# Optimization experiments

Hardware: AMD Instinct MI355X
Metric: run time of the kernel (lower is better)

Reference implementation:

```python
import jax, jax.numpy as jnp
import numpy as np

B, C, H, W = 4, 64, 64, 64  # x shape; mask is (B,1,8H,8W)


def _conv(x, w, pad=0):
    return jax.lax.conv_general_dilated(
        x, w, (1, 1), [(pad, pad), (pad, pad)],
        dimension_numbers=('NCHW', 'OIHW', 'NCHW'))


def _inorm(x, eps=1e-5):  # InstanceNorm2d, affine=False, biased var (torch default)
    mu = x.mean(axis=(2, 3), keepdims=True)
    var = x.var(axis=(2, 3), keepdims=True)
    return (x - mu) * jax.lax.rsqrt(var + eps)


def _forward(x, mask, kconv_w1, kconv_w2, fs_w1, fs_w2, fs_b2, fs_fuse_w):
    b, c, h, w = x.shape
    n = h * w
    # MaxPool2d(8,8) then binarize
    m = jax.lax.reduce_window(mask, -jnp.inf, jax.lax.max,
                              (1, 1, 8, 8), (1, 1, 8, 8), 'VALID')
    m = (m > 0).astype(x.dtype)
    back = 1.0 - m
    # ResidualBlock K_conv (shared for K and Q paths in original code)
    y = jax.nn.relu(_inorm(_conv(x, kconv_w1, pad=1)))
    y = _inorm(_conv(y, kconv_w2, pad=1))
    kx = jax.nn.relu(y + x)
    # L2-normalized K/Q over channel dim
    K = (kx * back).reshape(b, c, n)
    K = K / (jnp.linalg.norm(K, axis=1, keepdims=True) + 1e-8)
    Q = (kx * m).reshape(b, c, n)
    Q = Q / (jnp.linalg.norm(Q, axis=1, keepdims=True) + 1e-8)
    V = (x * back).reshape(b, c, n)
    # cosine-similarity score map, temperature 20
    score = jnp.einsum('bcq,bck->bqk', Q, K) * 20.0  # (b, n_q, n_k)
    qm = m.reshape(b, 1, n)      # query mask (foreground)
    km = back.reshape(b, 1, n)   # key mask (background)
    NEG = -1000000.0
    validx = score + (1.0 - km) * NEG + (1.0 - qm.transpose(0, 2, 1)) * NEG
    att = jax.nn.softmax(validx, axis=-1) * (qm.transpose(0, 2, 1) * km)
    # att_fore[b,c,q] = sum_k V[b,c,k] * att[b,q,k]
    att_fore = jnp.einsum('bck,bqk->bcq', V, att).reshape(b, c, h, w)
    # Fusion_score
    feat1 = _conv(jnp.concatenate([x * m, att_fore * m], axis=1), fs_w1)
    s = jax.nn.sigmoid(_conv(feat1, fs_w2) + fs_b2[None, :, None, None])
    fused = _conv(jnp.concatenate([x * m, att_fore * m * (1.0 - s)], axis=1), fs_fuse_w)
    fs_out = fused * m + x * (1.0 - m)
    out = fs_out * m + x * (1.0 - m)
    # visualization attention mask
    visatt = att.sum(axis=1).reshape(b, 1, h, w)
    attmask = jnp.repeat(jnp.repeat(visatt, 8, axis=2), 8, axis=3)  # nearest upsample x8
    attmask = attmask / attmask.max()
    return out, attmask


def setup_inputs() -> dict:
    key = jax.random.key(0)
    ks = jax.random.split(key, 8)

    def wgt(k, shape, fan_in):
        return jax.random.normal(k, shape, jnp.float32) / np.sqrt(fan_in)

    x = jax.random.normal(ks[0], (B, C, H, W), jnp.float32)
    # sparse foreground mask so maxpool(8x8)>0 yields a mixed fg/bg mask
    mask = (jax.random.uniform(ks[1], (B, 1, H * 8, W * 8)) < 0.01).astype(jnp.float32)
    return dict(
        x=x, mask=mask,
        kconv_w1=wgt(ks[2], (C, C, 3, 3), C * 9),
        kconv_w2=wgt(ks[3], (C, C, 3, 3), C * 9),
        fs_w1=wgt(ks[4], (C, 2 * C, 1, 1), 2 * C),
        fs_w2=wgt(ks[5], (C, C, 1, 1), C),
        fs_b2=jnp.zeros((C,), jnp.float32),
        fs_fuse_w=wgt(ks[6], (C, 2 * C, 1, 1), 2 * C),
    )


def reference(x, mask, kconv_w1, kconv_w2, fs_w1, fs_w2, fs_b2, fs_fuse_w):
    return _forward(x, mask, kconv_w1, kconv_w2, fs_w1, fs_w2, fs_b2, fs_fuse_w)
```

## Files before the change

### kernel.cpp

```cpp
#include <hip/hip_runtime.h>
#include <hip/hip_bf16.h>

typedef __hip_bfloat16 bf16;
typedef __attribute__((ext_vector_type(8))) short short8;
typedef __attribute__((ext_vector_type(4))) float f32x4;
typedef __attribute__((ext_vector_type(16))) float f32x16;

#define BB 4
#define CC 64
#define NN 4096
#define MH 512
#define MW 512
#define LS 72

#define WB_AFC  ((size_t)0)
#define WB_DEN  ((size_t)4194304)
#define WB_VIS  ((size_t)4259840)
#define WB_QIX  ((size_t)4325376)
#define WB_KIX  ((size_t)4390912)
#define WB_MFL  ((size_t)4456448)
#define WB_CNT  ((size_t)4472832)
#define WB_STAT ((size_t)4472896)
#define WB_WT1  ((size_t)4476992)
#define WB_WT2  ((size_t)4550720)
#define WB_WFB  ((size_t)4624448)

__device__ __forceinline__ float b2f(bf16 v) { return __bfloat162float(v); }
__device__ __forceinline__ float us2f(unsigned short u) { return __uint_as_float(((unsigned)u) << 16); }
__device__ __forceinline__ unsigned short f2bu(float f) {
  bf16 h = __float2bfloat16(f);
  return *(unsigned short*)&h;
}

__global__ __launch_bounds__(256) void k_maxpool(const float* __restrict__ mask,
                                                 unsigned char* __restrict__ mfl,
                                                 float* __restrict__ vis,
                                                 float* __restrict__ gstat,
                                                 unsigned int* __restrict__ vmaxb) {
  int g = blockIdx.x * 256 + threadIdx.x;
  int o = g >> 2, sub = g & 3;
  int b = o >> 12, p = o & 4095;
  int py = p >> 6, px = p & 63;
  const float* mb = mask + (size_t)b * MH * MW + (py * 8 + sub * 2) * MW + px * 8;
  float mx = 0.f;
  #pragma unroll
  for (int dy = 0; dy < 2; ++dy) {
    const float4* r4 = (const float4*)(mb + dy * MW);
    float4 a = r4[0], c = r4[1];
    mx = fmaxf(mx, fmaxf(fmaxf(a.x, a.y), fmaxf(a.z, a.w)));
    mx = fmaxf(mx, fmaxf(fmaxf(c.x, c.y), fmaxf(c.z, c.w)));
  }
  mx = fmaxf(mx, __shfl_xor(mx, 1));
  mx = fmaxf(mx, __shfl_xor(mx, 2));
  if (sub == 0) {
    mfl[o] = (mx > 0.f) ? 1 : 0;
    vis[o] = 0.f;
  }
  if (g < 1024) gstat[g] = 0.f;
  if (g == 0) vmaxb[0] = 0u;
}

__global__ __launch_bounds__(64) void k_compact(const unsigned char* __restrict__ mfl,
                                                int* __restrict__ qidx, int* __restrict__ kidx,
                                                int* __restrict__ nq, int* __restrict__ nk) {
  int b = blockIdx.x, lane = threadIdx.x;
  int qb = 0, kb = 0;
  for (int it = 0; it < 64; ++it) {
    int p = it * 64 + lane;
    bool f = mfl[b * NN + p] != 0;
    unsigned long long bal = __ballot(f);
    int before = __popcll(bal & ((1ULL << lane) - 1ULL));
    if (f)  qidx[b * NN + qb + before] = p;
    if (!f) kidx[b * NN + kb + (lane - before)] = p;
    int cnt = __popcll(bal);
    qb += cnt; kb += 64 - cnt;
  }
  if (lane == 0) { nq[b] = qb; nk[b] = kb; }
}

__global__ __launch_bounds__(256) void k_xT(const float* __restrict__ x,
                                            unsigned short* __restrict__ xt) {
  int b = blockIdx.x >> 6, p0 = (blockIdx.x & 63) * 64;
  __shared__ float lx[64][65];
  int t = threadIdx.x;
  const float* xb = x + (size_t)b * CC * NN + p0;
  for (int idx = t; idx < 4096; idx += 256) {
    int c = idx >> 6, j = idx & 63;
    lx[j][c] = xb[c * NN + j];
  }
  __syncthreads();
  unsigned short* xo = xt + ((size_t)b * NN + p0) * 64;
  for (int idx = t; idx < 2048; idx += 256) {
    int j = idx >> 5, c2 = (idx & 31) * 2;
    ushort2 w2;
    w2.x = f2bu(lx[j][c2]);
    w2.y = f2bu(lx[j][c2 + 1]);
    *(ushort2*)&xo[j * 64 + c2] = w2;
  }
}

__global__ __launch_bounds__(256) void k_wprep(const float* __restrict__ w1,
                                               const float* __restrict__ w2,
                                               const float* __restrict__ fw1,
                                               const float* __restrict__ fw2,
                                               const float* __restrict__ fwf,
                                               unsigned short* __restrict__ wT1,
                                               unsigned short* __restrict__ wT2,
                                               unsigned short* __restrict__ wfb) {
  int i = blockIdx.x * 256 + threadIdx.x;
  if (i < 36864) {
    int tap = i >> 12;
    int rem = i & 4095;
    int co = rem >> 6, ci = rem & 63;
    int src = (co * 64 + ci) * 9 + tap;
    wT1[i] = f2bu(w1[src]);
    wT2[i] = f2bu(w2[src]);
  } else if (i < 57344) {
    int j = i - 36864;
    if (j < 8192)       wfb[j] = f2bu(fw1[j]);
    else if (j < 12288) wfb[j] = f2bu(fw2[j - 8192]);
    else                wfb[j] = f2bu(fwf[j - 12288]);
  }
}

template <bool NORM_IN>
__global__ __launch_bounds__(256) void k_convm(const unsigned short* __restrict__ src,
                                               const unsigned short* __restrict__ wT,
                                               const float* __restrict__ insum,
                                               const float* __restrict__ insq,
                                               unsigned short* __restrict__ dst,
                                               float* __restrict__ gsum,
                                               float* __restrict__ gsq) {
  int b = blockIdx.y;
  int r = blockIdx.x;
  __shared__ unsigned short bx[198 * LS];
  __shared__ float nmean[64], ninv[64];
  int t = threadIdx.x;
  if (NORM_IN) {
    if (t < 64) {
      float m = insum[b * 64 + t] * (1.f / NN);
      float v = fmaxf(insq[b * 64 + t] * (1.f / NN) - m * m, 0.f);
      nmean[t] = m; ninv[t] = rsqrtf(v + 1e-5f);
    }
    __syncthreads();
  }
  const unsigned short* sb = src + (size_t)b * NN * 64;
  for (int idx = t; idx < 198 * 8; idx += 256) {
    int row = idx >> 3, c8 = (idx & 7) * 8;
    int dy = row / 66;
    int cx = row - dy * 66 - 1;
    int rr = r + dy - 1;
    uint4 v = make_uint4(0u, 0u, 0u, 0u);
    if ((unsigned)rr < 64u && (unsigned)cx < 64u) {
      v = *(const uint4*)(sb + ((size_t)(rr * 64 + cx)) * 64 + c8);
      if (NORM_IN) {
        unsigned short* e = (unsigned short*)&v;
        #pragma unroll
        for (int j = 0; j < 8; ++j)
          e[j] = f2bu(fmaxf((us2f(e[j]) - nmean[c8 + j]) * ninv[c8 + j], 0.f));
      }
    }
    *(uint4*)&bx[row * LS + c8] = v;
  }
  __syncthreads();
  int lane = t & 63;
  int quad = lane >> 4, col = lane & 15;
  int qw = (t >> 6) * 16;
  f32x4 acc[4] = {{0.f,0.f,0.f,0.f},{0.f,0.f,0.f,0.f},{0.f,0.f,0.f,0.f},{0.f,0.f,0.f,0.f}};
  #pragma unroll
  for (int tap = 0; tap < 9; ++tap) {
    int dy = tap / 3, dx = tap - dy * 3 - 1;
    const unsigned short* wrow = wT + ((size_t)tap * 64 + qw + col) * 64;
    short8 a0 = *(const short8*)(wrow + quad * 8);
    short8 a1 = *(const short8*)(wrow + 32 + quad * 8);
    int rbase = dy * 66 + dx + 1;
    #pragma unroll
    for (int nt = 0; nt < 4; ++nt) {
      int row = rbase + nt * 16 + col;
      short8 b0 = *(const short8*)&bx[row * LS + quad * 8];
      short8 b1 = *(const short8*)&bx[row * LS + 32 + quad * 8];
      acc[nt] = __builtin_amdgcn_mfma_f32_16x16x32_bf16(a0, b0, acc[nt], 0, 0, 0);
      acc[nt] = __builtin_amdgcn_mfma_f32_16x16x32_bf16(a1, b1, acc[nt], 0, 0, 0);
    }
  }
  #pragma unroll
  for (int rr = 0; rr < 4; ++rr) {
    float s1 = acc[0][rr] + acc[1][rr] + acc[2][rr] + acc[3][rr];
    float s2 = acc[0][rr]*acc[0][rr] + acc[1][rr]*acc[1][rr]
             + acc[2][rr]*acc[2][rr] + acc[3][rr]*acc[3][rr];
    s1 += __shfl_xor(s1, 1); s2 += __shfl_xor(s2, 1);
    s1 += __shfl_xor(s1, 2); s2 += __shfl_xor(s2, 2);
    s1 += __shfl_xor(s1, 4); s2 += __shfl_xor(s2, 4);
    s1 += __shfl_xor(s1, 8); s2 += __shfl_xor(s2, 8);
    if (col == 0) {
      int co = qw + quad * 4 + rr;
      atomicAdd(&gsum[b * 64 + co], s1);
      atomicAdd(&gsq[b * 64 + co], s2);
    }
  }
  __syncthreads();
  #pragma unroll
  for (int nt = 0; nt < 4; ++nt)
    #pragma unroll
    for (int rr = 0; rr < 4; ++rr)
      bx[(nt * 16 + col) * LS + qw + quad * 4 + rr] = f2bu(acc[nt][rr]);
  __syncthreads();
  unsigned short* db = dst + ((size_t)b * NN + r * 64) * 64;
  for (int idx = t; idx < 512; idx += 256) {
    int px = idx >> 3, c8 = (idx & 7) * 8;
    *(uint4*)(db + (size_t)px * 64 + c8) = *(const uint4*)&bx[px * LS + c8];
  }
}

__global__ __launch_bounds__(256) void k_knorm(unsigned short* __restrict__ kxt,
                                               const unsigned short* __restrict__ xt,
                                               const float* __restrict__ gsum,
                                               const float* __restrict__ gsq,
                                               float* __restrict__ afc,
                                               float* __restrict__ den) {
  int b = blockIdx.x >> 6;
  int p0 = (blockIdx.x & 63) * 64;
  __shared__ float m2[64], i2[64];
  int t = threadIdx.x;
  if (t < 64) {
    float m = gsum[b * 64 + t] * (1.f / NN);
    float v = fmaxf(gsq[b * 64 + t] * (1.f / NN) - m * m, 0.f);
    m2[t] = m; i2[t] = rsqrtf(v + 1e-5f);
  }
  size_t gid = (size_t)blockIdx.x * 256 + t;
  float4 z4 = make_float4(0.f, 0.f, 0.f, 0.f);
  float4* az = (float4*)afc;
  #pragma unroll
  for (int j = 0; j < 4; ++j) az[gid + (size_t)j * 65536] = z4;
  if (gid < 16384) den[gid] = 0.f;
  __syncthreads();
  int px = t >> 2, c0 = (t & 3) * 16;
  size_t base = ((size_t)b * NN + p0 + px) * 64 + c0;
  unsigned short kv[16], xv[16];
  *(uint4*)&kv[0] = *(const uint4*)(kxt + base);
  *(uint4*)&kv[8] = *(const uint4*)(kxt + base + 8);
  *(uint4*)&xv[0] = *(const uint4*)(xt + base);
  *(uint4*)&xv[8] = *(const uint4*)(xt + base + 8);
  float v[16]; float ss = 0.f;
  #pragma unroll
  for (int j = 0; j < 16; ++j) {
    float f = fmaxf((us2f(kv[j]) - m2[c0 + j]) * i2[c0 + j] + us2f(xv[j]), 0.f);
    v[j] = f; ss += f * f;
  }
  ss += __shfl_xor(ss, 1);
  ss += __shfl_xor(ss, 2);
  float inv = 1.f / (sqrtf(ss) + 1e-8f);
  #pragma unroll
  for (int j = 0; j < 16; ++j) kv[j] = f2bu(v[j] * inv);
  *(uint4*)(kxt + base) = *(const uint4*)&kv[0];
  *(uint4*)(kxt + base + 8) = *(const uint4*)&kv[8];
}

__global__ __launch_bounds__(256) void k_att1(const unsigned short* __restrict__ khat,
                                              const unsigned short* __restrict__ xt,
                                              const int* __restrict__ qidx, const int* __restrict__ kidx,
                                              const int* __restrict__ nqv, const int* __restrict__ nkv,
                                              float* __restrict__ afc, float* __restrict__ den) {
  int b = blockIdx.y;
  int nqb = nqv[b], nkb = nkv[b];
  int q0 = (blockIdx.x >> 3) * 64;
  int part = blockIdx.x & 7;
  if (q0 >= nqb) return;
  int kbeg = (part * nkb) >> 3;
  int kend = ((part + 1) * nkb) >> 3;
  __shared__ unsigned short lvT[64 * LS];
  __shared__ unsigned short le [64 * LS];
  int t = threadIdx.x;
  int wave = t >> 6, lane = t & 63;
  int l31 = lane & 31, lhi = lane >> 5;
  int qh = wave >> 1, kh = wave & 1;
  const int* qix = qidx + b * NN;
  const int* kix = kidx + b * NN;
  const unsigned short* khb = khat + (size_t)b * NN * 64;
  const unsigned short* xtb = xt + (size_t)b * NN * 64;
  int kix0 = kix[0];
  int qq_a = q0 + qh * 32 + l31;
  int qp_a = (qq_a < nqb) ? qix[qq_a] : qix[0];
  short8 aq[4];
  #pragma unroll
  for (int ks = 0; ks < 4; ++ks)
    aq[ks] = *(const short8*)(khb + (size_t)qp_a * 64 + ks * 16 + lhi * 8);
  f32x16 pv, dsum;
  #pragma unroll
  for (int i = 0; i < 16; ++i) { pv[i] = 0.f; dsum[i] = 0.f; }
  int kp2 = t >> 3, vc8 = (t & 7) * 8, vcc = (t & 7);
  for (int j0 = kbeg; j0 < kend; j0 += 64) {
    int krow = j0 + kh * 32 + l31;
    bool kval = krow < kend;
    int kp = kval ? kix[krow] : kix0;
    f32x16 s;
    #pragma unroll
    for (int i = 0; i < 16; ++i) s[i] = 0.f;
    #pragma unroll
    for (int ks = 0; ks < 4; ++ks) {
      short8 bk = *(const short8*)(khb + (size_t)kp * 64 + ks * 16 + lhi * 8);
      s = __builtin_amdgcn_mfma_f32_32x32x16_bf16(aq[ks], bk, s, 0, 0, 0);
    }
    __syncthreads();
    #pragma unroll
    for (int reg = 0; reg < 16; ++reg) {
      float e = kval ? __expf(20.f * s[reg]) : 0.f;
      dsum[reg] += e;
      int row = (reg & 3) + 8 * (reg >> 2) + 4 * lhi;
      le[(qh * 32 + row) * LS + kh * 32 + l31] = f2bu(e);
    }
    {
      uint4 v0 = make_uint4(0u, 0u, 0u, 0u);
      uint4 v1 = make_uint4(0u, 0u, 0u, 0u);
      int ka = j0 + 2 * kp2, kb2 = ka + 1;
      if (ka  < kend) v0 = *(const uint4*)(xtb + (size_t)kix[ka]  * 64 + vc8);
      if (kb2 < kend) v1 = *(const uint4*)(xtb + (size_t)kix[kb2] * 64 + vc8);
      const unsigned short* e0 = (const unsigned short*)&v0;
      const unsigned short* e1 = (const unsigned short*)&v1;
      int pbase = kp2 & 3, prun = kp2 >> 2;
      int pp = pbase + ((prun ^ vcc) << 2);
      #pragma unroll
      for (int jj = 0; jj < 8; ++jj) {
        int c = vc8 + jj;
        unsigned int w2 = (unsigned)e0[jj] | ((unsigned)e1[jj] << 16);
        *(unsigned int*)&lvT[c * LS + pp * 2] = w2;
      }
    }
    __syncthreads();
    int c = kh * 32 + l31;
    int c37 = (c >> 3) & 7;
    #pragma unroll
    for (int ks = 0; ks < 4; ++ks) {
      short8 a  = *(const short8*)&le[(qh * 32 + l31) * LS + ks * 16 + lhi * 8];
      int run = ks * 2 + lhi;
      short8 bv = *(const short8*)&lvT[c * LS + ((run ^ c37) << 3)];
      pv = __builtin_amdgcn_mfma_f32_32x32x16_bf16(a, bv, pv, 0, 0, 0);
    }
  }
  #pragma unroll
  for (int reg = 0; reg < 16; ++reg) {
    float v = dsum[reg];
    v += __shfl_xor(v, 1); v += __shfl_xor(v, 2); v += __shfl_xor(v, 4);
    v += __shfl_xor(v, 8); v += __shfl_xor(v, 16);
    int row = (reg & 3) + 8 * (reg >> 2) + 4 * lhi;
    int qq = q0 + qh * 32 + row;
    if (l31 == 0 && qq < nqb) atomicAdd(&den[b * NN + qq], v);
  }
  #pragma unroll
  for (int reg = 0; reg < 16; ++reg) {
    int row = (reg & 3) + 8 * (reg >> 2) + 4 * lhi;
    int qq = q0 + qh * 32 + row;
    if (qq < nqb) atomicAdd(&afc[((size_t)b * NN + qq) * 64 + kh * 32 + l31], pv[reg]);
  }
}

__global__ __launch_bounds__(256) void k_att2(const unsigned short* __restrict__ khat,
                                              const int* __restrict__ qidx, const int* __restrict__ kidx,
                                              const int* __restrict__ nqv, const int* __restrict__ nkv,
                                              const float* __restrict__ den, float* __restrict__ vis) {
  int b = blockIdx.y;
  int nqb = nqv[b], nkb = nkv[b];
  int k0 = (blockIdx.x >> 3) * 64;
  int part = blockIdx.x & 7;
  if (k0 >= nkb) return;
  int qbeg = (part * nqb) >> 3;
  int qend = ((part + 1) * nqb) >> 3;
  int t = threadIdx.x;
  int wave = t >> 6, lane = t & 63;
  int l31 = lane & 31, lhi = lane >> 5;
  int kh = wave >> 1, qh = wave & 1;
  const int* qix = qidx + b * NN;
  const int* kix = kidx + b * NN;
  const unsigned short* khb = khat + (size_t)b * NN * 64;
  int qix0 = qix[0];
  int kk_a = k0 + kh * 32 + l31;
  int kp_a = (kk_a < nkb) ? kix[kk_a] : kix[0];
  short8 ak[4];
  #pragma unroll
  for (int ks = 0; ks < 4; ++ks)
    ak[ks] = *(const short8*)(khb + (size_t)kp_a * 64 + ks * 16 + lhi * 8);
  f32x16 vacc;
  #pragma unroll
  for (int i = 0; i < 16; ++i) vacc[i] = 0.f;
  for (int i0 = qbeg; i0 < qend; i0 += 64) {
    int qrow = i0 + qh * 32 + l31;
    bool qv = qrow < qend;
    int qp = qv ? qix[qrow] : qix0;
    float d = qv ? den[b * NN + qrow] : 0.f;
    float wq = (d > 0.f) ? 1.f / d : 0.f;
    f32x16 s;
    #pragma unroll
    for (int i = 0; i < 16; ++i) s[i] = 0.f;
    #pragma unroll
    for (int ks = 0; ks < 4; ++ks) {
      short8 bq = *(const short8*)(khb + (size_t)qp * 64 + ks * 16 + lhi * 8);
      s = __builtin_amdgcn_mfma_f32_32x32x16_bf16(ak[ks], bq, s, 0, 0, 0);
    }
    #pragma unroll
    for (int reg = 0; reg < 16; ++reg) vacc[reg] += __expf(20.f * s[reg]) * wq;
  }
  #pragma unroll
  for (int reg = 0; reg < 16; ++reg) {
    float v = vacc[reg];
    v += __shfl_xor(v, 1); v += __shfl_xor(v, 2); v += __shfl_xor(v, 4);
    v += __shfl_xor(v, 8); v += __shfl_xor(v, 16);
    int row = (reg & 3) + 8 * (reg >> 2) + 4 * lhi;
    int kk = k0 + kh * 32 + row;
    if (l31 == 0 && kk < nkb) atomicAdd(&vis[b * NN + kix[kk]], v);
  }
}

__global__ __launch_bounds__(256) void k_copy(const uint4* __restrict__ src, uint4* __restrict__ dst, int n) {
  int i = blockIdx.x * 256 + threadIdx.x;
  if (i < n) dst[i] = src[i];
}

#define FS 136
__global__ __launch_bounds__(256) void k_fusionm(const unsigned short* __restrict__ xt,
                                                 const float* __restrict__ afc,
                                                 const float* __restrict__ den,
                                                 const int* __restrict__ qidx, const int* __restrict__ nqv,
                                                 const unsigned short* __restrict__ wall,
                                                 const float* __restrict__ b2,
                                                 float* __restrict__ outp) {
  int b = blockIdx.y;
  int nqb = nqv[b];
  int q0 = blockIdx.x * 64;
  if (q0 >= nqb) return;
  __shared__ unsigned short pxa[64 * FS];
  __shared__ unsigned short f1s[64 * LS];
  __shared__ int qpl[64];
  int t = threadIdx.x;
  int lane = t & 63;
  int quad = lane >> 4, col = lane & 15;
  int cb = (t >> 6) * 16;
  const int* qix = qidx + b * NN;
  const unsigned short* xtb = xt + (size_t)b * NN * 64;
  const unsigned short* w1b = wall;
  const unsigned short* w2b = wall + 8192;
  const unsigned short* wfb = wall + 12288;
  short8 a1[4], a2[2], af[4];
  #pragma unroll
  for (int kt = 0; kt < 4; ++kt) {
    a1[kt] = *(const short8*)&w1b[(cb + col) * 128 + kt * 32 + quad * 8];
    af[kt] = *(const short8*)&wfb[(cb + col) * 128 + kt * 32 + quad * 8];
  }
  #pragma unroll
  for (int kt = 0; kt < 2; ++kt)
    a2[kt] = *(const short8*)&w2b[(cb + col) * 64 + kt * 32 + quad * 8];
  float b2v[4];
  #pragma unroll
  for (int r = 0; r < 4; ++r) b2v[r] = b2[cb + quad * 4 + r];
  if (t < 64) qpl[t] = (q0 + t < nqb) ? qix[q0 + t] : -1;
  for (int idx = t; idx < 512; idx += 256) {
    int q = idx >> 3, c8 = (idx & 7) * 8;
    int qq = q0 + q;
    uint4 pv = make_uint4(0u, 0u, 0u, 0u);
    unsigned short pa8[8] = {0, 0, 0, 0, 0, 0, 0, 0};
    if (qq < nqb) {
      int qp = qix[qq];
      pv = *(const uint4*)(xtb + (size_t)qp * 64 + c8);
      float d = den[b * NN + qq];
      float invd = (d > 0.f) ? 1.f / d : 0.f;
      const float* ap = afc + ((size_t)b * NN + qq) * 64 + c8;
      #pragma unroll
      for (int j = 0; j < 8; ++j) pa8[j] = f2bu(ap[j] * invd);
    }
    *(uint4*)&pxa[q * FS + c8] = pv;
    *(uint4*)&pxa[q * FS + 64 + c8] = *(const uint4*)&pa8[0];
  }
  __syncthreads();
  #pragma unroll
  for (int qt = 0; qt < 4; ++qt) {
    f32x4 acc = {0.f, 0.f, 0.f, 0.f};
    #pragma unroll
    for (int kt = 0; kt < 4; ++kt) {
      short8 bfrag = *(const short8*)&pxa[(qt * 16 + col) * FS + kt * 32 + quad * 8];
      acc = __builtin_amdgcn_mfma_f32_16x16x32_bf16(a1[kt], bfrag, acc, 0, 0, 0);
    }
    #pragma unroll
    for (int r = 0; r < 4; ++r)
      f1s[(qt * 16 + col) * LS + cb + quad * 4 + r] = f2bu(acc[r]);
  }
  __syncthreads();
  #pragma unroll
  for (int qt = 0; qt < 4; ++qt) {
    f32x4 acc = {0.f, 0.f, 0.f, 0.f};
    #pragma unroll
    for (int kt = 0; kt < 2; ++kt) {
      short8 bfrag = *(const short8*)&f1s[(qt * 16 + col) * LS + kt * 32 + quad * 8];
      acc = __builtin_amdgcn_mfma_f32_16x16x32_bf16(a2[kt], bfrag, acc, 0, 0, 0);
    }
    #pragma unroll
    for (int r = 0; r < 4; ++r) {
      float sg = 1.f / (1.f + __expf(-(acc[r] + b2v[r])));
      int addr = (qt * 16 + col) * FS + 64 + cb + quad * 4 + r;
      pxa[addr] = f2bu(us2f(pxa[addr]) * (1.f - sg));
    }
  }
  __syncthreads();
  #pragma unroll
  for (int qt = 0; qt < 4; ++qt) {
    f32x4 acc = {0.f, 0.f, 0.f, 0.f};
    #pragma unroll
    for (int kt = 0; kt < 4; ++kt) {
      short8 bfrag = *(const short8*)&pxa[(qt * 16 + col) * FS + kt * 32 + quad * 8];
      acc = __builtin_amdgcn_mfma_f32_16x16x32_bf16(af[kt], bfrag, acc, 0, 0, 0);
    }
    int qp = qpl[qt * 16 + col];
    if (qp >= 0) {
      #pragma unroll
      for (int r = 0; r < 4; ++r)
        outp[((size_t)b * CC + cb + quad * 4 + r) * NN + qp] = acc[r];
    }
  }
}

__global__ __launch_bounds__(256) void k_vmax(const float* __restrict__ vis, unsigned int* __restrict__ vmaxb) {
  int i = blockIdx.x * 256 + threadIdx.x;
  float v = vis[i];
  #pragma unroll
  for (int off = 32; off > 0; off >>= 1) v = fmaxf(v, __shfl_down(v, off));
  if ((threadIdx.x & 63) == 0) atomicMax(vmaxb, __float_as_uint(v));
}

__global__ __launch_bounds__(256) void k_upsample(const float* __restrict__ vis,
                                                  const unsigned int* __restrict__ vmaxb,
                                                  float* __restrict__ out2) {
  int i = blockIdx.x * 256 + threadIdx.x;
  int b = i >> 18;
  int rem = i & 262143;
  int y = rem >> 9, x = rem & 511;
  float vm = __uint_as_float(vmaxb[0]);
  if (!(vm > 0.f)) vm = 1.f;
  out2[i] = vis[b * NN + (y >> 3) * 64 + (x >> 3)] / vm;
}

extern "C" void kernel_launch(void* const* d_in, const int* in_sizes, int n_in,
                              void* d_out, int out_size, void* d_ws, size_t ws_size,
                              hipStream_t stream) {
  const float* x    = (const float*)d_in[0];
  const float* mask = (const float*)d_in[1];
  const float* w1   = (const float*)d_in[2];
  const float* w2c  = (const float*)d_in[3];
  const float* fsw1 = (const float*)d_in[4];
  const float* fsw2 = (const float*)d_in[5];
  const float* fsb2 = (const float*)d_in[6];
  const float* fswf = (const float*)d_in[7];
  float* out = (float*)d_out;
  char* wsb = (char*)d_ws;

  float* afc = (float*)(wsb + WB_AFC);
  float* den = (float*)(wsb + WB_DEN);
  float* vis = (float*)(wsb + WB_VIS);
  int* qidx  = (int*)(wsb + WB_QIX);
  int* kidx  = (int*)(wsb + WB_KIX);
  unsigned char* mfl = (unsigned char*)(wsb + WB_MFL);
  int* nq = (int*)(wsb + WB_CNT);
  int* nk = nq + 4;
  unsigned int* vmaxb = (unsigned int*)(nq + 8);
  float* gstat = (float*)(wsb + WB_STAT);
  float* gsum1 = gstat;
  float* gsq1  = gstat + 256;
  float* gsum2 = gstat + 512;
  float* gsq2  = gstat + 768;
  unsigned short* wT1 = (unsigned short*)(wsb + WB_WT1);
  unsigned short* wT2 = (unsigned short*)(wsb + WB_WT2);
  unsigned short* wall = (unsigned short*)(wsb + WB_WFB);
  unsigned short* y1t = (unsigned short*)(wsb + WB_AFC);

  unsigned short* kxt = (unsigned short*)out;
  unsigned short* khat = kxt;
  unsigned short* xt = (unsigned short*)(out + 1048576);

  k_maxpool<<<256, 256, 0, stream>>>(mask, mfl, vis, gstat, vmaxb);
  k_compact<<<4, 64, 0, stream>>>(mfl, qidx, kidx, nq, nk);
  k_xT<<<256, 256, 0, stream>>>(x, xt);
  k_wprep<<<224, 256, 0, stream>>>(w1, w2c, fsw1, fsw2, fswf, wT1, wT2, wall);
  k_convm<false><<<dim3(64, BB), 256, 0, stream>>>(xt, wT1, nullptr, nullptr, y1t, gsum1, gsq1);
  k_convm<true><<<dim3(64, BB), 256, 0, stream>>>(y1t, wT2, gsum1, gsq1, kxt, gsum2, gsq2);
  k_knorm<<<256, 256, 0, stream>>>(kxt, xt, gsum2, gsq2, afc, den);
  k_att1<<<dim3(512, BB), 256, 0, stream>>>(khat, xt, qidx, kidx, nq, nk, afc, den);
  k_att2<<<dim3(512, BB), 256, 0, stream>>>(khat, qidx, kidx, nq, nk, den, vis);
  k_copy<<<1024, 256, 0, stream>>>((const uint4*)x, (uint4*)out, 262144);
  k_fusionm<<<dim3(64, BB), 256, 0, stream>>>(xt, afc, den, qidx, nq, wall, fsb2, out);
  k_vmax<<<64, 256, 0, stream>>>(vis, vmaxb);
  k_upsample<<<4096, 256, 0, stream>>>(vis, vmaxb, out + 1048576);
}
```

Baseline: 194.1 us.

## Merge prep kernels, parallelize compaction, split conv channels across more blocks

Folds maxpool, x transpose and weight prep into a single k_prep launch, and merges the vis max reduction with the output copy, cutting the number of kernel launches. Compaction now uses 1024 threads with a wave-level prefix scan instead of a single serial wave. Each conv is split into two output-channel halves per row, doubling the grid from 256 to 512 blocks for better CU occupancy, but each block now reloads the full halo tile for only half the work.

```diff
diff --git a/kernel.cpp b/kernel.cpp
--- a/kernel.cpp
+++ b/kernel.cpp
@@ -32,95 +32,116 @@
   return *(unsigned short*)&h;
 }
 
-__global__ __launch_bounds__(256) void k_maxpool(const float* __restrict__ mask,
-                                                 unsigned char* __restrict__ mfl,
-                                                 float* __restrict__ vis,
-                                                 float* __restrict__ gstat,
-                                                 unsigned int* __restrict__ vmaxb) {
-  int g = blockIdx.x * 256 + threadIdx.x;
-  int o = g >> 2, sub = g & 3;
-  int b = o >> 12, p = o & 4095;
-  int py = p >> 6, px = p & 63;
-  const float* mb = mask + (size_t)b * MH * MW + (py * 8 + sub * 2) * MW + px * 8;
-  float mx = 0.f;
-  #pragma unroll
-  for (int dy = 0; dy < 2; ++dy) {
-    const float4* r4 = (const float4*)(mb + dy * MW);
-    float4 a = r4[0], c = r4[1];
-    mx = fmaxf(mx, fmaxf(fmaxf(a.x, a.y), fmaxf(a.z, a.w)));
-    mx = fmaxf(mx, fmaxf(fmaxf(c.x, c.y), fmaxf(c.z, c.w)));
-  }
-  mx = fmaxf(mx, __shfl_xor(mx, 1));
-  mx = fmaxf(mx, __shfl_xor(mx, 2));
-  if (sub == 0) {
-    mfl[o] = (mx > 0.f) ? 1 : 0;
-    vis[o] = 0.f;
-  }
-  if (g < 1024) gstat[g] = 0.f;
-  if (g == 0) vmaxb[0] = 0u;
-}
-
-__global__ __launch_bounds__(64) void k_compact(const unsigned char* __restrict__ mfl,
-                                                int* __restrict__ qidx, int* __restrict__ kidx,
-                                                int* __restrict__ nq, int* __restrict__ nk) {
-  int b = blockIdx.x, lane = threadIdx.x;
-  int qb = 0, kb = 0;
-  for (int it = 0; it < 64; ++it) {
-    int p = it * 64 + lane;
-    bool f = mfl[b * NN + p] != 0;
-    unsigned long long bal = __ballot(f);
-    int before = __popcll(bal & ((1ULL << lane) - 1ULL));
-    if (f)  qidx[b * NN + qb + before] = p;
-    if (!f) kidx[b * NN + kb + (lane - before)] = p;
-    int cnt = __popcll(bal);
-    qb += cnt; kb += 64 - cnt;
-  }
-  if (lane == 0) { nq[b] = qb; nk[b] = kb; }
-}
-
-__global__ __launch_bounds__(256) void k_xT(const float* __restrict__ x,
-                                            unsigned short* __restrict__ xt) {
-  int b = blockIdx.x >> 6, p0 = (blockIdx.x & 63) * 64;
+__global__ __launch_bounds__(256) void k_prep(const float* __restrict__ mask,
+                                              const float* __restrict__ x,
+                                              const float* __restrict__ w1,
+                                              const float* __restrict__ w2,
+                                              const float* __restrict__ fw1,
+                                              const float* __restrict__ fw2,
+                                              const float* __restrict__ fwf,
+                                              unsigned char* __restrict__ mfl,
+                                              float* __restrict__ vis,
+                                              float* __restrict__ gstat,
+                                              unsigned int* __restrict__ vmaxb,
+                                              unsigned short* __restrict__ xt,
+                                              unsigned short* __restrict__ wT1,
+                                              unsigned short* __restrict__ wT2,
+                                              unsigned short* __restrict__ wfb) {
   __shared__ float lx[64][65];
-  int t = threadIdx.x;
-  const float* xb = x + (size_t)b * CC * NN + p0;
-  for (int idx = t; idx < 4096; idx += 256) {
-    int c = idx >> 6, j = idx & 63;
-    lx[j][c] = xb[c * NN + j];
-  }
-  __syncthreads();
-  unsigned short* xo = xt + ((size_t)b * NN + p0) * 64;
-  for (int idx = t; idx < 2048; idx += 256) {
-    int j = idx >> 5, c2 = (idx & 31) * 2;
-    ushort2 w2;
-    w2.x = f2bu(lx[j][c2]);
-    w2.y = f2bu(lx[j][c2 + 1]);
-    *(ushort2*)&xo[j * 64 + c2] = w2;
-  }
-}
-
-__global__ __launch_bounds__(256) void k_wprep(const float* __restrict__ w1,
-                                               const float* __restrict__ w2,
-                                               const float* __restrict__ fw1,
-                                               const float* __restrict__ fw2,
-                                               const float* __restrict__ fwf,
-                                               unsigned short* __restrict__ wT1,
-                                               unsigned short* __restrict__ wT2,
-                                               unsigned short* __restrict__ wfb) {
-  int i = blockIdx.x * 256 + threadIdx.x;
-  if (i < 36864) {
-    int tap = i >> 12;
-    int rem = i & 4095;
-    int co = rem >> 6, ci = rem & 63;
-    int src = (co * 64 + ci) * 9 + tap;
-    wT1[i] = f2bu(w1[src]);
-    wT2[i] = f2bu(w2[src]);
-  } else if (i < 57344) {
-    int j = i - 36864;
-    if (j < 8192)       wfb[j] = f2bu(fw1[j]);
-    else if (j < 12288) wfb[j] = f2bu(fw2[j - 8192]);
-    else                wfb[j] = f2bu(fwf[j - 12288]);
-  }
+  int bid = blockIdx.x;
+  int t = threadIdx.x;
+  if (bid < 256) {
+    int g = bid * 256 + t;
+    int o = g >> 2, sub = g & 3;
+    int b = o >> 12, p = o & 4095;
+    int py = p >> 6, px = p & 63;
+    const float* mb = mask + (size_t)b * MH * MW + (py * 8 + sub * 2) * MW + px * 8;
+    float mx = 0.f;
+    #pragma unroll
+    for (int dy = 0; dy < 2; ++dy) {
+      const float4* r4 = (const float4*)(mb + dy * MW);
+      float4 a = r4[0], c = r4[1];
+      mx = fmaxf(mx, fmaxf(fmaxf(a.x, a.y), fmaxf(a.z, a.w)));
+      mx = fmaxf(mx, fmaxf(fmaxf(c.x, c.y), fmaxf(c.z, c.w)));
+    }
+    mx = fmaxf(mx, __shfl_xor(mx, 1));
+    mx = fmaxf(mx, __shfl_xor(mx, 2));
+    if (sub == 0) {
+      mfl[o] = (mx > 0.f) ? 1 : 0;
+      vis[o] = 0.f;
+    }
+    if (g < 1024) gstat[g] = 0.f;
+    if (g == 0) vmaxb[0] = 0u;
+  } else if (bid < 512) {
+    int blk = bid - 256;
+    int b = blk >> 6, p0 = (blk & 63) * 64;
+    const float* xb = x + (size_t)b * CC * NN + p0;
+    for (int idx = t; idx < 4096; idx += 256) {
+      int c = idx >> 6, j = idx & 63;
+      lx[j][c] = xb[c * NN + j];
+    }
+    __syncthreads();
+    unsigned short* xo = xt + ((size_t)b * NN + p0) * 64;
+    for (int idx = t; idx < 2048; idx += 256) {
+      int j = idx >> 5, c2 = (idx & 31) * 2;
+      ushort2 w2v;
+      w2v.x = f2bu(lx[j][c2]);
+      w2v.y = f2bu(lx[j][c2 + 1]);
+      *(ushort2*)&xo[j * 64 + c2] = w2v;
+    }
+  } else {
+    int i = (bid - 512) * 256 + t;
+    if (i < 36864) {
+      int tap = i >> 12;
+      int rem = i & 4095;
+      int co = rem >> 6, ci = rem & 63;
+      int src = (co * 64 + ci) * 9 + tap;
+      wT1[i] = f2bu(w1[src]);
+      wT2[i] = f2bu(w2[src]);
+    } else if (i < 57344) {
+      int j = i - 36864;
+      if (j < 8192)       wfb[j] = f2bu(fw1[j]);
+      else if (j < 12288) wfb[j] = f2bu(fw2[j - 8192]);
+      else                wfb[j] = f2bu(fwf[j - 12288]);
+    }
+  }
+}
+
+__global__ __launch_bounds__(1024) void k_compact(const unsigned char* __restrict__ mfl,
+                                                  int* __restrict__ qidx, int* __restrict__ kidx,
+                                                  int* __restrict__ nq, int* __restrict__ nk) {
+  int b = blockIdx.x;
+  int t = threadIdx.x;
+  int lane = t & 63, w = t >> 6;
+  __shared__ int wtot[16], woff[16];
+  int p0 = t * 4;
+  const unsigned char* mb = mfl + b * NN;
+  uchar4 f4 = *(const uchar4*)&mb[p0];
+  int f0 = f4.x != 0, f1 = f4.y != 0, f2 = f4.z != 0, f3 = f4.w != 0;
+  int cnt = f0 + f1 + f2 + f3;
+  int inc = cnt;
+  #pragma unroll
+  for (int off = 1; off < 64; off <<= 1) {
+    int v = __shfl_up(inc, off);
+    if (lane >= off) inc += v;
+  }
+  if (lane == 63) wtot[w] = inc;
+  __syncthreads();
+  if (t == 0) {
+    int s = 0;
+    #pragma unroll
+    for (int i = 0; i < 16; ++i) { woff[i] = s; s += wtot[i]; }
+    nq[b] = s; nk[b] = NN - s;
+  }
+  __syncthreads();
+  int qp = woff[w] + inc - cnt;
+  int kp = p0 - qp;
+  int* qb = qidx + b * NN;
+  int* kb = kidx + b * NN;
+  if (f0) qb[qp++] = p0;     else kb[kp++] = p0;
+  if (f1) qb[qp++] = p0 + 1; else kb[kp++] = p0 + 1;
+  if (f2) qb[qp++] = p0 + 2; else kb[kp++] = p0 + 2;
+  if (f3) qb[qp++] = p0 + 3; else kb[kp++] = p0 + 3;
 }
 
 template <bool NORM_IN>
@@ -132,7 +153,8 @@
                                                float* __restrict__ gsum,
                                                float* __restrict__ gsq) {
   int b = blockIdx.y;
-  int r = blockIdx.x;
+  int r = blockIdx.x >> 1;
+  int half = blockIdx.x & 1;
   __shared__ unsigned short bx[198 * LS];
   __shared__ float nmean[64], ninv[64];
   int t = threadIdx.x;
@@ -165,18 +187,20 @@
   __syncthreads();
   int lane = t & 63;
   int quad = lane >> 4, col = lane & 15;
-  int qw = (t >> 6) * 16;
-  f32x4 acc[4] = {{0.f,0.f,0.f,0.f},{0.f,0.f,0.f,0.f},{0.f,0.f,0.f,0.f},{0.f,0.f,0.f,0.f}};
+  int w = t >> 6;
+  int nb = (w >> 1) * 2;
+  int cb = half * 32 + (w & 1) * 16;
+  f32x4 acc[2] = {{0.f,0.f,0.f,0.f},{0.f,0.f,0.f,0.f}};
   #pragma unroll
   for (int tap = 0; tap < 9; ++tap) {
     int dy = tap / 3, dx = tap - dy * 3 - 1;
-    const unsigned short* wrow = wT + ((size_t)tap * 64 + qw + col) * 64;
+    const unsigned short* wrow = wT + ((size_t)tap * 64 + cb + col) * 64;
     short8 a0 = *(const short8*)(wrow + quad * 8);
     short8 a1 = *(const short8*)(wrow + 32 + quad * 8);
     int rbase = dy * 66 + dx + 1;
     #pragma unroll
-    for (int nt = 0; nt < 4; ++nt) {
-      int row = rbase + nt * 16 + col;
+    for (int nt = 0; nt < 2; ++nt) {
+      int row = rbase + (nb + nt) * 16 + col;
       short8 b0 = *(const short8*)&bx[row * LS + quad * 8];
       short8 b1 = *(const short8*)&bx[row * LS + 32 + quad * 8];
       acc[nt] = __builtin_amdgcn_mfma_f32_16x16x32_bf16(a0, b0, acc[nt], 0, 0, 0);
@@ -185,29 +209,28 @@
   }
   #pragma unroll
   for (int rr = 0; rr < 4; ++rr) {
-    float s1 = acc[0][rr] + acc[1][rr] + acc[2][rr] + acc[3][rr];
-    float s2 = acc[0][rr]*acc[0][rr] + acc[1][rr]*acc[1][rr]
-             + acc[2][rr]*acc[2][rr] + acc[3][rr]*acc[3][rr];
+    float s1 = acc[0][rr] + acc[1][rr];
+    float s2 = acc[0][rr]*acc[0][rr] + acc[1][rr]*acc[1][rr];
     s1 += __shfl_xor(s1, 1); s2 += __shfl_xor(s2, 1);
     s1 += __shfl_xor(s1, 2); s2 += __shfl_xor(s2, 2);
     s1 += __shfl_xor(s1, 4); s2 += __shfl_xor(s2, 4);
     s1 += __shfl_xor(s1, 8); s2 += __shfl_xor(s2, 8);
     if (col == 0) {
-      int co = qw + quad * 4 + rr;
+      int co = cb + quad * 4 + rr;
       atomicAdd(&gsum[b * 64 + co], s1);
       atomicAdd(&gsq[b * 64 + co], s2);
     }
   }
   __syncthreads();
   #pragma unroll
-  for (int nt = 0; nt < 4; ++nt)
+  for (int nt = 0; nt < 2; ++nt)
     #pragma unroll
     for (int rr = 0; rr < 4; ++rr)
-      bx[(nt * 16 + col) * LS + qw + quad * 4 + rr] = f2bu(acc[nt][rr]);
-  __syncthreads();
-  unsigned short* db = dst + ((size_t)b * NN + r * 64) * 64;
-  for (int idx = t; idx < 512; idx += 256) {
-    int px = idx >> 3, c8 = (idx & 7) * 8;
+      bx[((nb + nt) * 16 + col) * LS + (w & 1) * 16 + quad * 4 + rr] = f2bu(acc[nt][rr]);
+  __syncthreads();
+  unsigned short* db = dst + ((size_t)b * NN + r * 64) * 64 + half * 32;
+  {
+    int px = t >> 2, c8 = (t & 3) * 8;
     *(uint4*)(db + (size_t)px * 64 + c8) = *(const uint4*)&bx[px * LS + c8];
   }
 }
@@ -410,9 +433,22 @@
   }
 }
 
-__global__ __launch_bounds__(256) void k_copy(const uint4* __restrict__ src, uint4* __restrict__ dst, int n) {
-  int i = blockIdx.x * 256 + threadIdx.x;
-  if (i < n) dst[i] = src[i];
+__global__ __launch_bounds__(256) void k_vmaxcopy(const float* __restrict__ vis,
+                                                  unsigned int* __restrict__ vmaxb,
+                                                  const uint4* __restrict__ src,
+                                                  uint4* __restrict__ dst) {
+  int bid = blockIdx.x;
+  int t = threadIdx.x;
+  if (bid < 64) {
+    int i = bid * 256 + t;
+    float v = vis[i];
+    #pragma unroll
+    for (int off = 32; off > 0; off >>= 1) v = fmaxf(v, __shfl_down(v, off));
+    if ((t & 63) == 0) atomicMax(vmaxb, __float_as_uint(v));
+  } else {
+    int i = (bid - 64) * 256 + t;
+    dst[i] = src[i];
+  }
 }
 
 #define FS 136
@@ -514,14 +550,6 @@
         outp[((size_t)b * CC + cb + quad * 4 + r) * NN + qp] = acc[r];
     }
   }
-}
-
-__global__ __launch_bounds__(256) void k_vmax(const float* __restrict__ vis, unsigned int* __restrict__ vmaxb) {
-  int i = blockIdx.x * 256 + threadIdx.x;
-  float v = vis[i];
-  #pragma unroll
-  for (int off = 32; off > 0; off >>= 1) v = fmaxf(v, __shfl_down(v, off));
-  if ((threadIdx.x & 63) == 0) atomicMax(vmaxb, __float_as_uint(v));
 }
 
 __global__ __launch_bounds__(256) void k_upsample(const float* __restrict__ vis,
@@ -573,17 +601,15 @@
   unsigned short* khat = kxt;
   unsigned short* xt = (unsigned short*)(out + 1048576);
 
-  k_maxpool<<<256, 256, 0, stream>>>(mask, mfl, vis, gstat, vmaxb);
-  k_compact<<<4, 64, 0, stream>>>(mfl, qidx, kidx, nq, nk);
-  k_xT<<<256, 256, 0, stream>>>(x, xt);
-  k_wprep<<<224, 256, 0, stream>>>(w1, w2c, fsw1, fsw2, fswf, wT1, wT2, wall);
-  k_convm<false><<<dim3(64, BB), 256, 0, stream>>>(xt, wT1, nullptr, nullptr, y1t, gsum1, gsq1);
-  k_convm<true><<<dim3(64, BB), 256, 0, stream>>>(y1t, wT2, gsum1, gsq1, kxt, gsum2, gsq2);
+  k_prep<<<736, 256, 0, stream>>>(mask, x, w1, w2c, fsw1, fsw2, fswf,
+                                  mfl, vis, gstat, vmaxb, xt, wT1, wT2, wall);
+  k_compact<<<4, 1024, 0, stream>>>(mfl, qidx, kidx, nq, nk);
+  k_convm<false><<<dim3(128, BB), 256, 0, stream>>>(xt, wT1, nullptr, nullptr, y1t, gsum1, gsq1);
+  k_convm<true><<<dim3(128, BB), 256, 0, stream>>>(y1t, wT2, gsum1, gsq1, kxt, gsum2, gsq2);
   k_knorm<<<256, 256, 0, stream>>>(kxt, xt, gsum2, gsq2, afc, den);
   k_att1<<<dim3(512, BB), 256, 0, stream>>>(khat, xt, qidx, kidx, nq, nk, afc, den);
   k_att2<<<dim3(512, BB), 256, 0, stream>>>(khat, qidx, kidx, nq, nk, den, vis);
-  k_copy<<<1024, 256, 0, stream>>>((const uint4*)x, (uint4*)out, 262144);
+  k_vmaxcopy<<<1088, 256, 0, stream>>>(vis, vmaxb, (const uint4*)x, (uint4*)out);
   k_fusionm<<<dim3(64, BB), 256, 0, stream>>>(xt, afc, den, qidx, nq, wall, fsb2, out);
-  k_vmax<<<64, 256, 0, stream>>>(vis, vmaxb);
   k_upsample<<<4096, 256, 0, stream>>>(vis, vmaxb, out + 1048576);
 }
```

Result: slower. 199.0 us (+2.5%).
